# Performance work log

Hardware: AMD Instinct MI355X
Metric: run time of the kernel (lower is better)

## Reference

```python
import jax, jax.numpy as jnp
import numpy as np

T = 2048            # flattened tokens (vLLM style)
D = 4096            # hidden_size
NSSM = 128          # ssm_state_size
K = 4               # conv kernel size
G = 8               # n_groups
H = 128             # mamba_num_heads
P = 64              # mamba_head_dim
INTER = H * P       # 8192 = expand * hidden_size
CONV_DIM = INTER + 2 * G * NSSM   # 10240 (x, B, C share the conv)
PROJ = INTER + CONV_DIM + H       # 18560 (z, xBC, dt)
Q = 128             # SSD chunk size
EPS = 1e-5


def setup_inputs() -> dict:
    key = jax.random.key(0)
    ks = jax.random.split(key, 9)
    s = 0.02
    return {
        "hidden_states": jax.random.normal(ks[0], (T, D), jnp.float32),
        "residual": jax.random.normal(ks[1], (T, D), jnp.float32),
        "norm_w": jnp.ones((D,), jnp.float32),
        "in_proj_w": jax.random.normal(ks[2], (PROJ, D), jnp.float32) * s,
        "conv_w": jax.random.normal(ks[3], (CONV_DIM, K), jnp.float32) * 0.2,
        "conv_b": jax.random.normal(ks[4], (CONV_DIM,), jnp.float32) * 0.1,
        "A_log": jnp.log(jax.random.uniform(ks[5], (H,), jnp.float32, 1.0, 16.0)),
        "D_res": jax.random.normal(ks[6], (H,), jnp.float32) * 0.5 + 1.0,
        "dt_bias": jax.random.normal(ks[7], (H,), jnp.float32) * 0.5,
        "gn_w": jnp.ones((INTER,), jnp.float32),
        "out_proj_w": jax.random.normal(ks[8], (D, INTER), jnp.float32) * s,
    }


def _forward(hidden_states, residual, norm_w, in_proj_w, conv_w, conv_b,
             A_log, D_res, dt_bias, gn_w, out_proj_w):
    # ---- fused add + RMSNorm (vLLM RMSNorm(hidden, residual)) ----
    resid = hidden_states + residual
    hs = resid * jax.lax.rsqrt(jnp.mean(resid * resid, -1, keepdims=True) + EPS) * norm_w

    # ---- MambaMixer2 ----
    proj = hs @ in_proj_w.T                              # [T, PROJ]
    z, xBC, dt = jnp.split(proj, [INTER, INTER + CONV_DIM], axis=-1)

    # causal depthwise conv1d over time + SiLU
    xp = jnp.pad(xBC, ((K - 1, 0), (0, 0)))
    conv = conv_b + sum(conv_w[:, k] * xp[k:k + T] for k in range(K))
    xBC = jax.nn.silu(conv)

    x, B, C = jnp.split(xBC, [INTER, INTER + G * NSSM], axis=-1)
    x = x.reshape(T, H, P)
    Bh = jnp.repeat(B.reshape(T, G, NSSM), H // G, axis=1)   # [T,H,N]
    Ch = jnp.repeat(C.reshape(T, G, NSSM), H // G, axis=1)   # [T,H,N]

    dt = jax.nn.softplus(dt + dt_bias)                   # [T,H]
    A = -jnp.exp(A_log)                                  # [H] (negative)

    # ---- SSD chunked selective scan ----
    NC = T // Q
    a = (dt * A).reshape(NC, Q, H)                       # per-step log decay (<=0)
    cum = jnp.cumsum(a, axis=1)                          # inclusive cumsum, [NC,Q,H]
    Xd = (dt[:, :, None] * x).reshape(NC, Q, H, P)
    Bc = Bh.reshape(NC, Q, H, NSSM)
    Cc = Ch.reshape(NC, Q, H, NSSM)

    # intra-chunk: Y[i] = sum_{j<=i} (C_i.B_j) exp(cum_i-cum_j) Xd_j
    CB = jnp.einsum('cqhn,ckhn->chqk', Cc, Bc)
    cumT = cum.transpose(0, 2, 1)                        # [NC,H,Q]
    mask = jnp.tril(jnp.ones((Q, Q), bool))
    Lm = jnp.where(mask, jnp.exp(cumT[:, :, :, None] - cumT[:, :, None, :]), 0.0)
    Y = jnp.einsum('chqk,ckhp->cqhp', CB * Lm, Xd)

    # chunk-local end states, then scan states across chunks
    cum_end = cum[:, -1]                                 # [NC,H]
    decay_out = jnp.exp(cum_end[:, None] - cum)          # [NC,Q,H]
    S_loc = jnp.einsum('cqhn,cqh,cqhp->chnp', Bc, decay_out, Xd)
    chunk_decay = jnp.exp(cum_end)                       # [NC,H]

    def step(s, inp):
        dec, sl = inp
        return dec[:, None, None] * s + sl, s            # emit state BEFORE chunk

    _, S_prev = jax.lax.scan(step, jnp.zeros((H, NSSM, P), x.dtype),
                             (chunk_decay, S_loc))       # [NC,H,N,P]

    # inter-chunk contribution + skip connection D*x
    Y = Y + jnp.einsum('cqhn,cqh,chnp->cqhp', Cc, jnp.exp(cum), S_prev)
    y = Y.reshape(T, H, P) + D_res[None, :, None] * x

    # gated RMSNorm then out projection
    y = y.reshape(T, INTER) * jax.nn.silu(z)
    y = y * jax.lax.rsqrt(jnp.mean(y * y, -1, keepdims=True) + EPS) * gn_w
    return y @ out_proj_w.T, resid


def reference(hidden_states, residual, norm_w, in_proj_w, conv_w, conv_b,
              A_log, D_res, dt_bias, gn_w, out_proj_w):
    return _forward(hidden_states, residual, norm_w, in_proj_w, conv_w, conv_b,
                    A_log, D_res, dt_bias, gn_w, out_proj_w)
```

## Files before the change

### kernel.cpp

```cpp
#include <hip/hip_runtime.h>
#include <stdint.h>

typedef unsigned short u16;
typedef unsigned int   u32;
typedef float  f32x4  __attribute__((ext_vector_type(4)));
typedef __bf16 bf16x8 __attribute__((ext_vector_type(8)));
typedef u16    u16x4  __attribute__((ext_vector_type(4)));
typedef u16    u16x8  __attribute__((ext_vector_type(8)));

#define T_N     2048
#define D_N     4096
#define H_N     128
#define P_N     64
#define G_N     8
#define NS_N    128
#define INTER_N 8192
#define CONVD_N 10240
#define PROJ_N  18560
#define NGEMM_N 18432
#define NC_N    16

__device__ __forceinline__ float bf2f(u16 u){ u32 x = ((u32)u) << 16; return __builtin_bit_cast(float, x); }
__device__ __forceinline__ u16 f2bf(float f){
  u32 u = __builtin_bit_cast(u32, f);
  u += 0x7FFFu + ((u >> 16) & 1u);
  return (u16)(u >> 16);
}

__device__ __forceinline__ void gld_lds16(const void* g, void* lds){
  __builtin_amdgcn_global_load_lds(
      (const __attribute__((address_space(1))) void*)(uintptr_t)g,
      (__attribute__((address_space(3))) void*)(u32)(uintptr_t)lds,
      16, 0, 0);
}

__global__ __launch_bounds__(256)
void k_addnorm(const float* __restrict__ hin, const float* __restrict__ rin,
               const float* __restrict__ nw, float* __restrict__ resid,
               u16* __restrict__ hs16, float* __restrict__ rstd){
  __shared__ float red[4];
  const int row = blockIdx.x, tid = threadIdx.x;
  const size_t rb = (size_t)row * D_N;
  f32x4 s[4];
  float ss = 0.f;
  #pragma unroll
  for (int i = 0; i < 4; ++i){
    int c4 = tid + i*256;
    f32x4 a = *(const f32x4*)&hin[rb + (size_t)c4*4];
    f32x4 b = *(const f32x4*)&rin[rb + (size_t)c4*4];
    s[i] = a + b;
    *(f32x4*)&resid[rb + (size_t)c4*4] = s[i];
    ss += s[i][0]*s[i][0] + s[i][1]*s[i][1] + s[i][2]*s[i][2] + s[i][3]*s[i][3];
  }
  #pragma unroll
  for (int o = 32; o > 0; o >>= 1) ss += __shfl_down(ss, o, 64);
  if ((tid & 63) == 0) red[tid >> 6] = ss;
  __syncthreads();
  float tot = (red[0] + red[1]) + (red[2] + red[3]);
  float rs = rsqrtf(tot / (float)D_N + 1e-5f);
  if (tid == 0) rstd[row] = rs;
  #pragma unroll
  for (int i = 0; i < 4; ++i){
    int c4 = tid + i*256;
    f32x4 w = *(const f32x4*)&nw[(size_t)c4*4];
    u16x4 o = { f2bf(s[i][0]*rs*w[0]), f2bf(s[i][1]*rs*w[1]),
                f2bf(s[i][2]*rs*w[2]), f2bf(s[i][3]*rs*w[3]) };
    *(u16x4*)&hs16[rb + (size_t)c4*4] = o;
  }
}

__global__ void k_cvt(const float* __restrict__ in, u16* __restrict__ out, size_t n4){
  size_t i = (size_t)blockIdx.x * blockDim.x + threadIdx.x;
  size_t stride = (size_t)gridDim.x * blockDim.x;
  for (; i < n4; i += stride){
    f32x4 v = *(const f32x4*)&in[i*4];
    u16x4 o = { f2bf(v[0]), f2bf(v[1]), f2bf(v[2]), f2bf(v[3]) };
    *(u16x4*)&out[i*4] = o;
  }
}

__global__ void k_wdt(const float* __restrict__ W, const float* __restrict__ nw,
                      float* __restrict__ Wn){
  int idx = blockIdx.x*256 + threadIdx.x;
  int d = idx >> 7, h = idx & 127;
  Wn[(size_t)d*128 + h] = W[(size_t)(INTER_N + CONVD_N + h)*D_N + d] * nw[d];
}

__global__ __launch_bounds__(256)
void k_dtgemm(const float* __restrict__ resid, const float* __restrict__ Wn,
              float* __restrict__ dtpart){
  __shared__ float lhs[16*128];
  const int tid = threadIdx.x;
  const int tb = blockIdx.x >> 3, ks = blockIdx.x & 7;
  const int t0 = tb * 16;
  const int k0 = ks * (D_N / 8);
  const int hcol = tid & 127, rh = tid >> 7;
  float acc[8] = {0,0,0,0,0,0,0,0};
  for (int kt = k0; kt < k0 + D_N/8; kt += 128){
    __syncthreads();
    #pragma unroll
    for (int it = 0; it < 2; ++it){
      int idx = it*256 + tid;
      int rr = idx >> 5, c4 = idx & 31;
      *(f32x4*)&lhs[rr*128 + c4*4] = *(const f32x4*)&resid[(size_t)(t0+rr)*D_N + kt + c4*4];
    }
    __syncthreads();
    #pragma unroll 4
    for (int kk4 = 0; kk4 < 32; ++kk4){
      f32x4 w4;
      #pragma unroll
      for (int j = 0; j < 4; ++j) w4[j] = Wn[(size_t)(kt + kk4*4 + j)*128 + hcol];
      #pragma unroll
      for (int j = 0; j < 8; ++j){
        f32x4 lv = *(const f32x4*)&lhs[(rh*8 + j)*128 + kk4*4];
        acc[j] += lv[0]*w4[0] + lv[1]*w4[1] + lv[2]*w4[2] + lv[3]*w4[3];
      }
    }
  }
  #pragma unroll
  for (int j = 0; j < 8; ++j){
    int t = t0 + rh*8 + j;
    dtpart[((size_t)ks*T_N + t)*128 + hcol] = acc[j];
  }
}

__global__ void k_dtprep(const float* __restrict__ dtpart, const float* __restrict__ rstd,
                         const float* __restrict__ dt_bias, const float* __restrict__ A_log,
                         float* __restrict__ dtv, float* __restrict__ cum,
                         float* __restrict__ cumend, float* __restrict__ dec){
  int c = blockIdx.x, h = threadIdx.x;
  float A = -expf(A_log[h]);
  float bias = dt_bias[h];
  float cm = 0.f;
  for (int q = 0; q < 128; ++q){
    int t = c*128 + q;
    float s = 0.f;
    #pragma unroll
    for (int kspl = 0; kspl < 8; ++kspl)
      s += dtpart[((size_t)kspl*T_N + t)*128 + h];
    float x = s * rstd[t] + bias;
    float dv = (x > 20.f) ? x : log1pf(expf(x));
    dtv[(size_t)t*128 + h] = dv;
    cm += dv * A;
    cum[(size_t)t*128 + h] = cm;
  }
  cumend[c*128 + h] = cm;
  dec[c*128 + h] = expf(cm);
}

#define STA(BUF,HH,KT) gld_lds16(pA + (size_t)((HH)*64)*K + (size_t)(KT)*64, shb + (BUF)*BSZ + (HH)*8192 + tid*16)
#define STB(BUF,HH,KT) gld_lds16(pB[HH] + (size_t)(KT)*64, shb + (BUF)*BSZ + 32768 + (HH)*8192 + tid*16)
#define VMWN do { asm volatile("s_waitcnt vmcnt(%0)" :: "n"(NFRAG) : "memory"); __builtin_amdgcn_sched_barrier(0); } while(0)
#define RDA(BUF, Q, V0, V1, V2, V3)                                                     \
    bf16x8 V0 = *(const bf16x8*)(shb + (BUF)*BSZ + rdA + (Q)*4096 + sA0);               \
    bf16x8 V1 = *(const bf16x8*)(shb + (BUF)*BSZ + rdA + (Q)*4096 + sA1);               \
    bf16x8 V2 = *(const bf16x8*)(shb + (BUF)*BSZ + rdA + (Q)*4096 + 2048 + sA0);        \
    bf16x8 V3 = *(const bf16x8*)(shb + (BUF)*BSZ + rdA + (Q)*4096 + 2048 + sA1);
#define RDB(BUF, BB)                                                                    \
    _Pragma("unroll") for (int nn = 0; nn < NFRAG; ++nn){                               \
      BB[nn][0] = *(const bf16x8*)(shb + (BUF)*BSZ + rdB + nn*2048 + sA0);              \
      BB[nn][1] = *(const bf16x8*)(shb + (BUF)*BSZ + rdB + nn*2048 + sA1);              \
    }
#define MM8(Q, V0, V1, V2, V3, BB)                                                      \
    _Pragma("unroll") for (int nn = 0; nn < NFRAG; ++nn){                               \
      acc[(Q)*2+0][nn] = __builtin_amdgcn_mfma_f32_16x16x32_bf16(V0, BB[nn][0], acc[(Q)*2+0][nn],0,0,0); \
      acc[(Q)*2+0][nn] = __builtin_amdgcn_mfma_f32_16x16x32_bf16(V1, BB[nn][1], acc[(Q)*2+0][nn],0,0,0); \
      acc[(Q)*2+1][nn] = __builtin_amdgcn_mfma_f32_16x16x32_bf16(V2, BB[nn][0], acc[(Q)*2+1][nn],0,0,0); \
      acc[(Q)*2+1][nn] = __builtin_amdgcn_mfma_f32_16x16x32_bf16(V3, BB[nn][1], acc[(Q)*2+1][nn],0,0,0); \
    }
#define ENDPH                                                                           \
    __builtin_amdgcn_s_setprio(0);                                                      \
    __builtin_amdgcn_s_barrier();                                                       \
    __builtin_amdgcn_sched_barrier(0);

template<int NFRAG, typename OT>
__global__ __launch_bounds__(512, 2)
void k_gemm256(const u16* __restrict__ A, const u16* __restrict__ Bm,
               OT* __restrict__ C, int ldc, int K, int nkt, size_t zstride){
  constexpr int BSZ = 32768 + NFRAG*8192;
  __shared__ char shb[2*BSZ];
  const int tid = threadIdx.x, ln = tid & 63, wid = tid >> 6;
  const int wm = wid >> 2, wn = wid & 3;
  const int lr = ln & 15, lg = ln >> 4;

  const int gx = gridDim.x;
  const int lin = blockIdx.y * gx + blockIdx.x;
  const int xcd = lin & 7, sub = lin >> 3;
  const int ncx = gx >> 3;
  const int m0 = (sub / ncx) << 8;
  const int n0 = (xcd * ncx + (sub % ncx)) * (NFRAG*64);
  const int kbase = blockIdx.z * nkt;

  const int srow = tid >> 3;
  const int slog = ((tid & 7) ^ (srow & 7)) * 8;
  const u16* pA = A + (size_t)(m0 + srow)*K + (size_t)kbase*64 + slog;
  const u16* pB[NFRAG];
  #pragma unroll
  for (int hh = 0; hh < NFRAG; ++hh)
    pB[hh] = Bm + (size_t)(n0 + hh*64 + srow)*K + (size_t)kbase*64 + slog;

  const int sA0 = (lg ^ (ln & 7)) << 4;
  const int sA1 = ((4 + lg) ^ (ln & 7)) << 4;
  const u32 rdA = wm*16384 + lr*128;
  const u32 rdB = 32768 + (wn*NFRAG*16 + lr)*128;

  f32x4 acc[8][NFRAG] = {};

  #pragma unroll
  for (int hh = 0; hh < 4; ++hh) STA(0, hh, 0);
  #pragma unroll
  for (int hh = 0; hh < NFRAG; ++hh) STB(0, hh, 0);
  #pragma unroll
  for (int hh = 0; hh < NFRAG; ++hh) STB(1, hh, 1);
  VMWN;
  __builtin_amdgcn_s_barrier();
  __builtin_amdgcn_sched_barrier(0);

  const int nit = nkt >> 1;
  #pragma unroll 1
  for (int it = 0; it < nit; ++it){
    const int t1 = 2*it + 1;
    int t2 = 2*it + 2; if (t2 >= nkt) t2 = 0;
    int t3 = 2*it + 3; if (t3 >= nkt) t3 = 1;
    bf16x8 bb0[NFRAG][2], bb1[NFRAG][2];
    {
      RDA(0,0, x0,x1,x2,x3) RDA(0,1, y0,y1,y2,y3) RDB(0, bb0)
      #pragma unroll
      for (int hh = 0; hh < 4; ++hh) STA(1, hh, t1);
      __builtin_amdgcn_s_setprio(1);
      MM8(0, x0,x1,x2,x3, bb0)
      MM8(1, y0,y1,y2,y3, bb0)
      ENDPH
    }
    {
      RDA(0,2, x0,x1,x2,x3) RDA(0,3, y0,y1,y2,y3)
      #pragma unroll
      for (int hh = 0; hh < NFRAG; ++hh) STB(0, hh, t2);
      VMWN;
      __builtin_amdgcn_s_setprio(1);
      MM8(2, x0,x1,x2,x3, bb0)
      MM8(3, y0,y1,y2,y3, bb0)
      ENDPH
    }
    {
      RDA(1,0, x0,x1,x2,x3) RDA(1,1, y0,y1,y2,y3) RDB(1, bb1)
      #pragma unroll
      for (int hh = 0; hh < 4; ++hh) STA(0, hh, t2);
      __builtin_amdgcn_s_setprio(1);
      MM8(0, x0,x1,x2,x3, bb1)
      MM8(1, y0,y1,y2,y3, bb1)
      ENDPH
    }
    {
      RDA(1,2, x0,x1,x2,x3) RDA(1,3, y0,y1,y2,y3)
      #pragma unroll
      for (int hh = 0; hh < NFRAG; ++hh) STB(1, hh, t3);
      VMWN;
      __builtin_amdgcn_s_setprio(1);
      MM8(2, x0,x1,x2,x3, bb1)
      MM8(3, y0,y1,y2,y3, bb1)
      ENDPH
    }
  }
  asm volatile("s_waitcnt vmcnt(0)" ::: "memory");

  OT* Cz = C + (size_t)blockIdx.z * zstride;
  const int crow = m0 + wm*128 + lg*4;
  const int ccol = n0 + wn*(NFRAG*16) + lr;
  #pragma unroll
  for (int m = 0; m < 8; ++m)
    #pragma unroll
    for (int nn = 0; nn < NFRAG; ++nn)
      #pragma unroll
      for (int r = 0; r < 4; ++r){
        float v = acc[m][nn][r];
        if constexpr (__is_same(OT, float))
          Cz[(size_t)(crow + m*16 + r)*ldc + ccol + nn*16] = v;
        else
          Cz[(size_t)(crow + m*16 + r)*ldc + ccol + nn*16] = f2bf(v);
      }
}

__global__ __launch_bounds__(256)
void k_add2(const float* __restrict__ a, const float* __restrict__ b,
            float* __restrict__ o, int n4){
  int i = blockIdx.x*256 + threadIdx.x;
  if (i < n4){
    f32x4 x = *(const f32x4*)&a[(size_t)i*4];
    f32x4 y = *(const f32x4*)&b[(size_t)i*4];
    x = x + y;
    *(f32x4*)&o[(size_t)i*4] = x;
  }
}

__global__ __launch_bounds__(256)
void k_conv(const u16* __restrict__ proj16, const float* __restrict__ cw,
            const float* __restrict__ cb, u16* __restrict__ x16,
            u16* __restrict__ B16, u16* __restrict__ C16){
  const int ch = blockIdx.x*256 + threadIdx.x;
  const int tbase = blockIdx.y*64;
  f32x4 w = *(const f32x4*)&cw[(size_t)ch*4];
  const float bias = cb[ch];
  const u16* pcol = proj16 + INTER_N + ch;
  float p0 = 0.f, p1 = 0.f, p2 = 0.f;
  if (tbase >= 3){
    p0 = bf2f(pcol[(size_t)(tbase-3)*PROJ_N]);
    p1 = bf2f(pcol[(size_t)(tbase-2)*PROJ_N]);
    p2 = bf2f(pcol[(size_t)(tbase-1)*PROJ_N]);
  }
  u16* xdst = (ch < INTER_N) ? x16 + ch
            : (ch < INTER_N + 1024) ? B16 + (ch - INTER_N)
            : C16 + (ch - INTER_N - 1024);
  const int dstride = (ch < INTER_N) ? INTER_N : 1024;
  #pragma unroll 4
  for (int i = 0; i < 64; ++i){
    int t = tbase + i;
    float cur = bf2f(pcol[(size_t)t*PROJ_N]);
    float acc = bias + w[0]*p0 + w[1]*p1 + w[2]*p2 + w[3]*cur;
    float v = acc / (1.f + __expf(-acc));
    xdst[(size_t)t*dstride] = f2bf(v);
    p0 = p1; p1 = p2; p2 = cur;
  }
}

__global__ __launch_bounds__(512)
void k_ssda(const u16* __restrict__ B16, const u16* __restrict__ x16,
            const float* __restrict__ dtv, const float* __restrict__ cum,
            const float* __restrict__ cumend, u16* __restrict__ SlocT){
  __shared__ u16 lBdT[128*136];
  __shared__ u16 lXdT[64*136];
  __shared__ float lDec[128], lDt[128];
  const int tid = threadIdx.x, wid = tid >> 6, ln = tid & 63;
  const int c = blockIdx.x >> 7, h = blockIdx.x & 127, g = h >> 4;
  if (tid < 128){
    int t = c*128 + tid;
    lDec[tid] = __expf(cumend[c*128 + h] - cum[(size_t)t*128 + h]);
    lDt[tid]  = dtv[(size_t)t*128 + h];
  }
  __syncthreads();
  for (int it = 0; it < 32; ++it){
    int idx = it*512 + tid;
    int q = idx >> 7, n = idx & 127;
    float bv = bf2f(B16[(size_t)(c*128 + q)*1024 + g*128 + n]) * lDec[q];
    lBdT[n*136 + q] = f2bf(bv);
  }
  for (int it = 0; it < 16; ++it){
    int idx = it*512 + tid;
    int q = idx >> 6, p = idx & 63;
    float xv = bf2f(x16[(size_t)(c*128 + q)*INTER_N + h*64 + p]) * lDt[q];
    lXdT[p*136 + q] = f2bf(xv);
  }
  __syncthreads();
  const int wr = wid >> 1, wc = wid & 1;
  const int kofs = (ln >> 4) << 3;
  f32x4 acc[2][2] = {};
  #pragma unroll
  for (int ks = 0; ks < 4; ++ks){
    bf16x8 a[2], b[2];
    #pragma unroll
    for (int m = 0; m < 2; ++m) a[m] = *(const bf16x8*)&lBdT[(wr*32 + m*16 + (ln & 15))*136 + ks*32 + kofs];
    #pragma unroll
    for (int n = 0; n < 2; ++n) b[n] = *(const bf16x8*)&lXdT[(wc*32 + n*16 + (ln & 15))*136 + ks*32 + kofs];
    #pragma unroll
    for (int m = 0; m < 2; ++m)
      #pragma unroll
      for (int n = 0; n < 2; ++n)
        acc[m][n] = __builtin_amdgcn_mfma_f32_16x16x32_bf16(a[m], b[n], acc[m][n], 0, 0, 0);
  }
  const size_t base = (size_t)(c*128 + h) * 8192;
  #pragma unroll
  for (int m = 0; m < 2; ++m)
    #pragma unroll
    for (int n = 0; n < 2; ++n){
      int p  = wc*32 + n*16 + (ln & 15);
      int nn = wr*32 + m*16 + ((ln >> 4) << 2);
      u16x4 o = { f2bf(acc[m][n][0]), f2bf(acc[m][n][1]), f2bf(acc[m][n][2]), f2bf(acc[m][n][3]) };
      *(u16x4*)&SlocT[base + (size_t)p*128 + nn] = o;
    }
}

__global__ __launch_bounds__(256)
void k_scan(const u16* __restrict__ SlocT, const float* __restrict__ dec,
            u16* __restrict__ SprevT){
  int idx = blockIdx.x*256 + threadIdx.x;
  int h = idx >> 11, p = (idx >> 5) & 63, n4 = idx & 31;
  float s0 = 0.f, s1 = 0.f, s2 = 0.f, s3 = 0.f;
  for (int c = 0; c < NC_N; ++c){
    size_t off = (size_t)(c*128 + h)*8192 + (size_t)p*128 + n4*4;
    u16x4 o = { f2bf(s0), f2bf(s1), f2bf(s2), f2bf(s3) };
    *(u16x4*)&SprevT[off] = o;
    u16x4 sl = *(const u16x4*)&SlocT[off];
    float d = dec[c*128 + h];
    s0 = d*s0 + bf2f(sl[0]); s1 = d*s1 + bf2f(sl[1]);
    s2 = d*s2 + bf2f(sl[2]); s3 = d*s3 + bf2f(sl[3]);
  }
}

__global__ __launch_bounds__(512)
void k_ssdb(const u16* __restrict__ C16, const u16* __restrict__ B16g,
            const u16* __restrict__ x16, const float* __restrict__ dtv,
            const float* __restrict__ cum, const u16* __restrict__ SprevT,
            const u16* __restrict__ proj16, const float* __restrict__ Dres,
            u16* __restrict__ yg16){
  __shared__ u16 lC[128*136];
  __shared__ u16 lBP[128*136];
  __shared__ u16 lXdT[64*136];
  __shared__ float lCum[128], lDt[128];
  const int tid = threadIdx.x, wid = tid >> 6, ln = tid & 63;
  const int c = blockIdx.x >> 7, h = blockIdx.x & 127, g = h >> 4;
  if (tid < 128){
    int t = c*128 + tid;
    lCum[tid] = cum[(size_t)t*128 + h];
    lDt[tid]  = dtv[(size_t)t*128 + h];
  }
  __syncthreads();
  for (int it = 0; it < 32; ++it){
    int idx = it*512 + tid;
    int q = idx >> 7, n = idx & 127;
    size_t gi = (size_t)(c*128 + q)*1024 + g*128 + n;
    lC[q*136 + n]  = C16[gi];
    lBP[q*136 + n] = B16g[gi];
  }
  for (int it = 0; it < 16; ++it){
    int idx = it*512 + tid;
    int q = idx >> 6, p = idx & 63;
    lXdT[p*136 + q] = f2bf(bf2f(x16[(size_t)(c*128 + q)*INTER_N + h*64 + p]) * lDt[q]);
  }
  __syncthreads();
  const int kofs = (ln >> 4) << 3;
  {
    const int wr = wid >> 2, wc = wid & 3;
    f32x4 cb[4][2] = {};
    #pragma unroll
    for (int ks = 0; ks < 4; ++ks){
      bf16x8 a[4], b[2];
      #pragma unroll
      for (int m = 0; m < 4; ++m) a[m] = *(const bf16x8*)&lC[(wr*64 + m*16 + (ln & 15))*136 + ks*32 + kofs];
      #pragma unroll
      for (int n = 0; n < 2; ++n) b[n] = *(const bf16x8*)&lBP[(wc*32 + n*16 + (ln & 15))*136 + ks*32 + kofs];
      #pragma unroll
      for (int m = 0; m < 4; ++m)
        #pragma unroll
        for (int n = 0; n < 2; ++n)
          cb[m][n] = __builtin_amdgcn_mfma_f32_16x16x32_bf16(a[m], b[n], cb[m][n], 0, 0, 0);
    }
    __syncthreads();
    #pragma unroll
    for (int m = 0; m < 4; ++m)
      #pragma unroll
      for (int n = 0; n < 2; ++n){
        int kcol = (wid & 3)*32 + n*16 + (ln & 15);
        float ck = lCum[kcol];
        #pragma unroll
        for (int r = 0; r < 4; ++r){
          int q = (wid >> 2)*64 + m*16 + ((ln >> 4) << 2) + r;
          float v = (kcol <= q) ? cb[m][n][r] * __expf(lCum[q] - ck) : 0.f;
          lBP[q*136 + kcol] = f2bf(v);
        }
      }
  }
  __syncthreads();
  const int yr = wid >> 1, yc = wid & 1;
  f32x4 y1[2][2] = {}, y2[2][2] = {};
  const size_t spbase = (size_t)(c*128 + h) * 8192;
  #pragma unroll
  for (int ks = 0; ks < 4; ++ks){
    bf16x8 ap[2], acf[2], bx[2], bs[2];
    #pragma unroll
    for (int m = 0; m < 2; ++m){
      int qr = yr*32 + m*16 + (ln & 15);
      ap[m]  = *(const bf16x8*)&lBP[qr*136 + ks*32 + kofs];
      acf[m] = *(const bf16x8*)&lC [qr*136 + ks*32 + kofs];
    }
    #pragma unroll
    for (int n = 0; n < 2; ++n){
      int p = yc*32 + n*16 + (ln & 15);
      bx[n] = *(const bf16x8*)&lXdT[p*136 + ks*32 + kofs];
      bs[n] = *(const bf16x8*)&SprevT[spbase + (size_t)p*128 + ks*32 + kofs];
    }
    #pragma unroll
    for (int m = 0; m < 2; ++m)
      #pragma unroll
      for (int n = 0; n < 2; ++n){
        y1[m][n] = __builtin_amdgcn_mfma_f32_16x16x32_bf16(ap[m],  bx[n], y1[m][n], 0, 0, 0);
        y2[m][n] = __builtin_amdgcn_mfma_f32_16x16x32_bf16(acf[m], bs[n], y2[m][n], 0, 0, 0);
      }
  }
  const float dh = Dres[h];
  #pragma unroll
  for (int m = 0; m < 2; ++m)
    #pragma unroll
    for (int r = 0; r < 4; ++r){
      int q = yr*32 + m*16 + ((ln >> 4) << 2) + r;
      float eq = __expf(lCum[q]);
      size_t t = (size_t)(c*128 + q);
      #pragma unroll
      for (int n = 0; n < 2; ++n){
        int p = yc*32 + n*16 + (ln & 15);
        int chn = h*64 + p;
        float xv = bf2f(x16[t*INTER_N + chn]);
        float zv = bf2f(proj16[t*PROJ_N + chn]);
        float yv = y1[m][n][r] + eq*y2[m][n][r] + dh*xv;
        float sg = zv / (1.f + __expf(-zv));
        yg16[t*INTER_N + chn] = f2bf(yv * sg);
      }
    }
}

__global__ __launch_bounds__(256)
void k_gnorm(const u16* __restrict__ yg, const float* __restrict__ gnw,
             u16* __restrict__ yn16){
  __shared__ float red[4];
  const int row = blockIdx.x, tid = threadIdx.x;
  const u16* rp = yg + (size_t)row * INTER_N;
  u16x8 v[4];
  float ss = 0.f;
  #pragma unroll
  for (int i = 0; i < 4; ++i){
    v[i] = *(const u16x8*)&rp[(size_t)(tid + i*256)*8];
    #pragma unroll
    for (int j = 0; j < 8; ++j){ float f = bf2f(v[i][j]); ss += f*f; }
  }
  #pragma unroll
  for (int o = 32; o > 0; o >>= 1) ss += __shfl_down(ss, o, 64);
  if ((tid & 63) == 0) red[tid >> 6] = ss;
  __syncthreads();
  float tot = (red[0] + red[1]) + (red[2] + red[3]);
  float sc = rsqrtf(tot / (float)INTER_N + 1e-5f);
  #pragma unroll
  for (int i = 0; i < 4; ++i){
    int c8 = (tid + i*256)*8;
    u16x8 o;
    #pragma unroll
    for (int j = 0; j < 8; ++j)
      o[j] = f2bf(bf2f(v[i][j]) * sc * gnw[c8 + j]);
    *(u16x8*)&yn16[(size_t)row*INTER_N + c8] = o;
  }
}

extern "C" void kernel_launch(void* const* d_in, const int* in_sizes, int n_in,
                              void* d_out, int out_size, void* d_ws, size_t ws_size,
                              hipStream_t stream){
  (void)in_sizes; (void)n_in; (void)out_size;
  const float* hs_in     = (const float*)d_in[0];
  const float* res_in    = (const float*)d_in[1];
  const float* norm_w    = (const float*)d_in[2];
  const float* in_proj_w = (const float*)d_in[3];
  const float* conv_w    = (const float*)d_in[4];
  const float* conv_b    = (const float*)d_in[5];
  const float* A_log     = (const float*)d_in[6];
  const float* D_res     = (const float*)d_in[7];
  const float* dt_bias   = (const float*)d_in[8];
  const float* gn_w      = (const float*)d_in[9];
  const float* out_proj_w= (const float*)d_in[10];

  float* out0      = (float*)d_out;
  float* resid_out = out0 + (size_t)T_N * D_N;

  char* ws = (char*)d_ws;
  const size_t o_hs16   = 0;
  const size_t o_Win16  = 16777216;
  const size_t o_Wout16 = 168820736;
  const size_t o_proj   = 235929600;
  const size_t o_plane  = 311951360;
  const size_t o_Wn     = 387973120;
  const size_t o_dtv    = 391118848;
  const size_t o_cum    = 392167424;
  const size_t o_cumend = 393216000;
  const size_t o_dec    = 393224192;
  const size_t o_rstd   = 393232384;
  const size_t o_x16    = 393240576;
  const size_t o_B16    = 426795008;
  const size_t o_C16    = 430989312;
  const size_t o_SlocT  = 435183616;
  const size_t o_SprevT = 468738048;
  const size_t o_yn16   = 502292480;
  const size_t WS_NEED  = 535846912;
  if (ws_size < WS_NEED) return;

  u16*   hs16   = (u16*)  (ws + o_hs16);
  u16*   Win16  = (u16*)  (ws + o_Win16);
  u16*   Wout16 = (u16*)  (ws + o_Wout16);
  u16*   proj16 = (u16*)  (ws + o_proj);
  float* planes = (float*)(ws + o_plane);
  float* Wn     = (float*)(ws + o_Wn);
  float* dtpart = (float*)(ws + o_proj);
  float* dtv    = (float*)(ws + o_dtv);
  float* cum    = (float*)(ws + o_cum);
  float* cumend = (float*)(ws + o_cumend);
  float* dec    = (float*)(ws + o_dec);
  float* rstd   = (float*)(ws + o_rstd);
  u16*   x16    = (u16*)  (ws + o_x16);
  u16*   B16    = (u16*)  (ws + o_B16);
  u16*   C16    = (u16*)  (ws + o_C16);
  u16*   SlocT  = (u16*)  (ws + o_SlocT);
  u16*   SprevT = (u16*)  (ws + o_SprevT);
  u16*   yn16   = (u16*)  (ws + o_yn16);
  u16*   yg16   = (u16*)  (ws + o_Win16);

  k_addnorm<<<T_N, 256, 0, stream>>>(hs_in, res_in, norm_w, resid_out, hs16, rstd);
  k_cvt<<<4096, 256, 0, stream>>>(in_proj_w,  Win16,  (size_t)NGEMM_N * D_N / 4);
  k_cvt<<<2048, 256, 0, stream>>>(out_proj_w, Wout16, (size_t)D_N * INTER_N / 4);
  k_wdt<<<2048, 256, 0, stream>>>(in_proj_w, norm_w, Wn);
  k_dtgemm<<<1024, 256, 0, stream>>>(resid_out, Wn, dtpart);
  k_dtprep<<<NC_N, 128, 0, stream>>>(dtpart, rstd, dt_bias, A_log, dtv, cum, cumend, dec);
  k_gemm256<3, u16><<<dim3(NGEMM_N/192, T_N/256, 1), 512, 0, stream>>>(hs16, Win16, proj16, PROJ_N, D_N, D_N/64, 0);
  k_conv<<<dim3(CONVD_N/256, T_N/64), 256, 0, stream>>>(proj16, conv_w, conv_b, x16, B16, C16);
  k_ssda<<<NC_N * H_N, 512, 0, stream>>>(B16, x16, dtv, cum, cumend, SlocT);
  k_scan<<<1024, 256, 0, stream>>>(SlocT, dec, SprevT);
  k_ssdb<<<NC_N * H_N, 512, 0, stream>>>(C16, B16, x16, dtv, cum, SprevT, proj16, D_res, yg16);
  k_gnorm<<<T_N, 256, 0, stream>>>(yg16, gn_w, yn16);
  k_gemm256<4, float><<<dim3(D_N/256, T_N/256, 2), 512, 0, stream>>>(yn16, Wout16, planes, D_N, INTER_N, INTER_N/64/2, (size_t)T_N*D_N);
  k_add2<<<T_N*D_N/1024, 256, 0, stream>>>(planes, planes + (size_t)T_N*D_N, out0, T_N*D_N/4);
}
```

Baseline: 952.6 us.

## Shrink GEMM tiles to 128 rows and drop split-K for out projection

The shared GEMM kernel's M tile drops from 256 to 128 rows, which halves the A staging in LDS and the accumulator registers, and the occupancy hint rises from 2 to 4 blocks. The output projection no longer uses split-K with two fp32 partial planes and a separate add kernel. It now runs as a single pass with NFRAG=2 (128x128 tiles) and writes straight to the output. The aim is more blocks in flight and no extra plane writes or reduction kernel, at the cost of less data reuse per tile and more A/B reloads.

```diff
diff --git a/kernel.cpp b/kernel.cpp
--- a/kernel.cpp
+++ b/kernel.cpp
@@ -149,7 +149,7 @@
 }
 
 #define STA(BUF,HH,KT) gld_lds16(pA + (size_t)((HH)*64)*K + (size_t)(KT)*64, shb + (BUF)*BSZ + (HH)*8192 + tid*16)
-#define STB(BUF,HH,KT) gld_lds16(pB[HH] + (size_t)(KT)*64, shb + (BUF)*BSZ + 32768 + (HH)*8192 + tid*16)
+#define STB(BUF,HH,KT) gld_lds16(pB[HH] + (size_t)(KT)*64, shb + (BUF)*BSZ + 16384 + (HH)*8192 + tid*16)
 #define VMWN do { asm volatile("s_waitcnt vmcnt(%0)" :: "n"(NFRAG) : "memory"); __builtin_amdgcn_sched_barrier(0); } while(0)
 #define RDA(BUF, Q, V0, V1, V2, V3)                                                     \
     bf16x8 V0 = *(const bf16x8*)(shb + (BUF)*BSZ + rdA + (Q)*4096 + sA0);               \
@@ -174,10 +174,10 @@
     __builtin_amdgcn_sched_barrier(0);
 
 template<int NFRAG, typename OT>
-__global__ __launch_bounds__(512, 2)
+__global__ __launch_bounds__(512, 4)
 void k_gemm256(const u16* __restrict__ A, const u16* __restrict__ Bm,
-               OT* __restrict__ C, int ldc, int K, int nkt, size_t zstride){
-  constexpr int BSZ = 32768 + NFRAG*8192;
+               OT* __restrict__ C, int ldc, int K, int nkt){
+  constexpr int BSZ = 16384 + NFRAG*8192;
   __shared__ char shb[2*BSZ];
   const int tid = threadIdx.x, ln = tid & 63, wid = tid >> 6;
   const int wm = wid >> 2, wn = wid & 3;
@@ -187,27 +187,25 @@
   const int lin = blockIdx.y * gx + blockIdx.x;
   const int xcd = lin & 7, sub = lin >> 3;
   const int ncx = gx >> 3;
-  const int m0 = (sub / ncx) << 8;
+  const int m0 = (sub / ncx) << 7;
   const int n0 = (xcd * ncx + (sub % ncx)) * (NFRAG*64);
-  const int kbase = blockIdx.z * nkt;
 
   const int srow = tid >> 3;
   const int slog = ((tid & 7) ^ (srow & 7)) * 8;
-  const u16* pA = A + (size_t)(m0 + srow)*K + (size_t)kbase*64 + slog;
+  const u16* pA = A + (size_t)(m0 + srow)*K + slog;
   const u16* pB[NFRAG];
   #pragma unroll
   for (int hh = 0; hh < NFRAG; ++hh)
-    pB[hh] = Bm + (size_t)(n0 + hh*64 + srow)*K + (size_t)kbase*64 + slog;
+    pB[hh] = Bm + (size_t)(n0 + hh*64 + srow)*K + slog;
 
   const int sA0 = (lg ^ (ln & 7)) << 4;
   const int sA1 = ((4 + lg) ^ (ln & 7)) << 4;
-  const u32 rdA = wm*16384 + lr*128;
-  const u32 rdB = 32768 + (wn*NFRAG*16 + lr)*128;
-
-  f32x4 acc[8][NFRAG] = {};
-
-  #pragma unroll
-  for (int hh = 0; hh < 4; ++hh) STA(0, hh, 0);
+  const u32 rdA = wm*8192 + lr*128;
+  const u32 rdB = 16384 + (wn*NFRAG*16 + lr)*128;
+
+  f32x4 acc[4][NFRAG] = {};
+
+  STA(0, 0, 0); STA(0, 1, 0);
   #pragma unroll
   for (int hh = 0; hh < NFRAG; ++hh) STB(0, hh, 0);
   #pragma unroll
@@ -224,73 +222,54 @@
     int t3 = 2*it + 3; if (t3 >= nkt) t3 = 1;
     bf16x8 bb0[NFRAG][2], bb1[NFRAG][2];
     {
-      RDA(0,0, x0,x1,x2,x3) RDA(0,1, y0,y1,y2,y3) RDB(0, bb0)
-      #pragma unroll
-      for (int hh = 0; hh < 4; ++hh) STA(1, hh, t1);
+      RDA(0,0, x0,x1,x2,x3) RDB(0, bb0)
+      STA(1, 0, t1); STA(1, 1, t1);
       __builtin_amdgcn_s_setprio(1);
       MM8(0, x0,x1,x2,x3, bb0)
-      MM8(1, y0,y1,y2,y3, bb0)
       ENDPH
     }
     {
-      RDA(0,2, x0,x1,x2,x3) RDA(0,3, y0,y1,y2,y3)
+      RDA(0,1, x0,x1,x2,x3)
       #pragma unroll
       for (int hh = 0; hh < NFRAG; ++hh) STB(0, hh, t2);
       VMWN;
       __builtin_amdgcn_s_setprio(1);
-      MM8(2, x0,x1,x2,x3, bb0)
-      MM8(3, y0,y1,y2,y3, bb0)
+      MM8(1, x0,x1,x2,x3, bb0)
       ENDPH
     }
     {
-      RDA(1,0, x0,x1,x2,x3) RDA(1,1, y0,y1,y2,y3) RDB(1, bb1)
-      #pragma unroll
-      for (int hh = 0; hh < 4; ++hh) STA(0, hh, t2);
+      RDA(1,0, x0,x1,x2,x3) RDB(1, bb1)
+      STA(0, 0, t2); STA(0, 1, t2);
       __builtin_amdgcn_s_setprio(1);
       MM8(0, x0,x1,x2,x3, bb1)
-      MM8(1, y0,y1,y2,y3, bb1)
       ENDPH
     }
     {
-      RDA(1,2, x0,x1,x2,x3) RDA(1,3, y0,y1,y2,y3)
+      RDA(1,1, x0,x1,x2,x3)
       #pragma unroll
       for (int hh = 0; hh < NFRAG; ++hh) STB(1, hh, t3);
       VMWN;
       __builtin_amdgcn_s_setprio(1);
-      MM8(2, x0,x1,x2,x3, bb1)
-      MM8(3, y0,y1,y2,y3, bb1)
+      MM8(1, x0,x1,x2,x3, bb1)
       ENDPH
     }
   }
   asm volatile("s_waitcnt vmcnt(0)" ::: "memory");
 
-  OT* Cz = C + (size_t)blockIdx.z * zstride;
-  const int crow = m0 + wm*128 + lg*4;
+  const int crow = m0 + wm*64 + lg*4;
   const int ccol = n0 + wn*(NFRAG*16) + lr;
   #pragma unroll
-  for (int m = 0; m < 8; ++m)
+  for (int m = 0; m < 4; ++m)
     #pragma unroll
     for (int nn = 0; nn < NFRAG; ++nn)
       #pragma unroll
       for (int r = 0; r < 4; ++r){
         float v = acc[m][nn][r];
         if constexpr (__is_same(OT, float))
-          Cz[(size_t)(crow + m*16 + r)*ldc + ccol + nn*16] = v;
+          C[(size_t)(crow + m*16 + r)*ldc + ccol + nn*16] = v;
         else
-          Cz[(size_t)(crow + m*16 + r)*ldc + ccol + nn*16] = f2bf(v);
+          C[(size_t)(crow + m*16 + r)*ldc + ccol + nn*16] = f2bf(v);
       }
-}
-
-__global__ __launch_bounds__(256)
-void k_add2(const float* __restrict__ a, const float* __restrict__ b,
-            float* __restrict__ o, int n4){
-  int i = blockIdx.x*256 + threadIdx.x;
-  if (i < n4){
-    f32x4 x = *(const f32x4*)&a[(size_t)i*4];
-    f32x4 y = *(const f32x4*)&b[(size_t)i*4];
-    x = x + y;
-    *(f32x4*)&o[(size_t)i*4] = x;
-  }
 }
 
 __global__ __launch_bounds__(256)
@@ -562,7 +541,6 @@
   const size_t o_Win16  = 16777216;
   const size_t o_Wout16 = 168820736;
   const size_t o_proj   = 235929600;
-  const size_t o_plane  = 311951360;
   const size_t o_Wn     = 387973120;
   const size_t o_dtv    = 391118848;
   const size_t o_cum    = 392167424;
@@ -582,7 +560,6 @@
   u16*   Win16  = (u16*)  (ws + o_Win16);
   u16*   Wout16 = (u16*)  (ws + o_Wout16);
   u16*   proj16 = (u16*)  (ws + o_proj);
-  float* planes = (float*)(ws + o_plane);
   float* Wn     = (float*)(ws + o_Wn);
   float* dtpart = (float*)(ws + o_proj);
   float* dtv    = (float*)(ws + o_dtv);
@@ -604,12 +581,11 @@
   k_wdt<<<2048, 256, 0, stream>>>(in_proj_w, norm_w, Wn);
   k_dtgemm<<<1024, 256, 0, stream>>>(resid_out, Wn, dtpart);
   k_dtprep<<<NC_N, 128, 0, stream>>>(dtpart, rstd, dt_bias, A_log, dtv, cum, cumend, dec);
-  k_gemm256<3, u16><<<dim3(NGEMM_N/192, T_N/256, 1), 512, 0, stream>>>(hs16, Win16, proj16, PROJ_N, D_N, D_N/64, 0);
+  k_gemm256<3, u16><<<dim3(NGEMM_N/192, T_N/128), 512, 0, stream>>>(hs16, Win16, proj16, PROJ_N, D_N, D_N/64);
   k_conv<<<dim3(CONVD_N/256, T_N/64), 256, 0, stream>>>(proj16, conv_w, conv_b, x16, B16, C16);
   k_ssda<<<NC_N * H_N, 512, 0, stream>>>(B16, x16, dtv, cum, cumend, SlocT);
   k_scan<<<1024, 256, 0, stream>>>(SlocT, dec, SprevT);
   k_ssdb<<<NC_N * H_N, 512, 0, stream>>>(C16, B16, x16, dtv, cum, SprevT, proj16, D_res, yg16);
   k_gnorm<<<T_N, 256, 0, stream>>>(yg16, gn_w, yn16);
-  k_gemm256<4, float><<<dim3(D_N/256, T_N/256, 2), 512, 0, stream>>>(yn16, Wout16, planes, D_N, INTER_N, INTER_N/64/2, (size_t)T_N*D_N);
-  k_add2<<<T_N*D_N/1024, 256, 0, stream>>>(planes, planes + (size_t)T_N*D_N, out0, T_N*D_N/4);
-}
+  k_gemm256<2, float><<<dim3(D_N/128, T_N/128), 512, 0, stream>>>(yn16, Wout16, out0, D_N, INTER_N, INTER_N/64);
+}
```

Result: no change. 947.4 us (-0.5%).

## Replace 256-wide GEMM with 256x128 tile, K=32 step, 4-wave kernel

Applied to the files above, without the earlier changes.

Both bf16 GEMMs move from a 512-thread kernel with 256xN (N=192/256) tiles and K-step 64 to a 256-thread kernel with 256x128 tiles and K-step 32, using smaller LDS buffers and a new swizzle and block remapping. The intent is higher occupancy and more blocks per GEMM for better CU balance, at the cost of lower arithmetic intensity per tile and twice as many barriers per K. The out-projection split-K planes now alias the proj workspace, which is no longer needed by then.

```diff
diff --git a/kernel.cpp b/kernel.cpp
--- a/kernel.cpp
+++ b/kernel.cpp
@@ -148,73 +148,58 @@
   dec[c*128 + h] = expf(cm);
 }
 
-#define STA(BUF,HH,KT) gld_lds16(pA + (size_t)((HH)*64)*K + (size_t)(KT)*64, shb + (BUF)*BSZ + (HH)*8192 + tid*16)
-#define STB(BUF,HH,KT) gld_lds16(pB[HH] + (size_t)(KT)*64, shb + (BUF)*BSZ + 32768 + (HH)*8192 + tid*16)
-#define VMWN do { asm volatile("s_waitcnt vmcnt(%0)" :: "n"(NFRAG) : "memory"); __builtin_amdgcn_sched_barrier(0); } while(0)
-#define RDA(BUF, Q, V0, V1, V2, V3)                                                     \
-    bf16x8 V0 = *(const bf16x8*)(shb + (BUF)*BSZ + rdA + (Q)*4096 + sA0);               \
-    bf16x8 V1 = *(const bf16x8*)(shb + (BUF)*BSZ + rdA + (Q)*4096 + sA1);               \
-    bf16x8 V2 = *(const bf16x8*)(shb + (BUF)*BSZ + rdA + (Q)*4096 + 2048 + sA0);        \
-    bf16x8 V3 = *(const bf16x8*)(shb + (BUF)*BSZ + rdA + (Q)*4096 + 2048 + sA1);
-#define RDB(BUF, BB)                                                                    \
-    _Pragma("unroll") for (int nn = 0; nn < NFRAG; ++nn){                               \
-      BB[nn][0] = *(const bf16x8*)(shb + (BUF)*BSZ + rdB + nn*2048 + sA0);              \
-      BB[nn][1] = *(const bf16x8*)(shb + (BUF)*BSZ + rdB + nn*2048 + sA1);              \
-    }
-#define MM8(Q, V0, V1, V2, V3, BB)                                                      \
-    _Pragma("unroll") for (int nn = 0; nn < NFRAG; ++nn){                               \
-      acc[(Q)*2+0][nn] = __builtin_amdgcn_mfma_f32_16x16x32_bf16(V0, BB[nn][0], acc[(Q)*2+0][nn],0,0,0); \
-      acc[(Q)*2+0][nn] = __builtin_amdgcn_mfma_f32_16x16x32_bf16(V1, BB[nn][1], acc[(Q)*2+0][nn],0,0,0); \
-      acc[(Q)*2+1][nn] = __builtin_amdgcn_mfma_f32_16x16x32_bf16(V2, BB[nn][0], acc[(Q)*2+1][nn],0,0,0); \
-      acc[(Q)*2+1][nn] = __builtin_amdgcn_mfma_f32_16x16x32_bf16(V3, BB[nn][1], acc[(Q)*2+1][nn],0,0,0); \
-    }
-#define ENDPH                                                                           \
-    __builtin_amdgcn_s_setprio(0);                                                      \
-    __builtin_amdgcn_s_barrier();                                                       \
-    __builtin_amdgcn_sched_barrier(0);
-
-template<int NFRAG, typename OT>
-__global__ __launch_bounds__(512, 2)
-void k_gemm256(const u16* __restrict__ A, const u16* __restrict__ Bm,
-               OT* __restrict__ C, int ldc, int K, int nkt, size_t zstride){
-  constexpr int BSZ = 32768 + NFRAG*8192;
+#define STA(BUF,HH,KT) gld_lds16(pA + (size_t)((HH)*64)*K + (size_t)(KT)*32, shb + (BUF)*BSZ + (HH)*4096 + tid*16)
+#define STB(BUF,HH,KT) gld_lds16(pB + (size_t)((HH)*64)*K + (size_t)(KT)*32, shb + (BUF)*BSZ + 16384 + (HH)*4096 + tid*16)
+#define VMW2 do { asm volatile("s_waitcnt vmcnt(2)" ::: "memory"); __builtin_amdgcn_sched_barrier(0); } while(0)
+#define BAR  do { __builtin_amdgcn_s_barrier(); __builtin_amdgcn_sched_barrier(0); } while(0)
+#define RDAF(BUF, MOFF, AA)                                                             \
+    _Pragma("unroll") for (int mm = 0; mm < 4; ++mm)                                    \
+      AA[mm] = *(const bf16x8*)(shb + (BUF)*BSZ + rdA + ((MOFF)+mm)*1024 + sxor);
+#define RDBF(BUF, BB)                                                                   \
+    _Pragma("unroll") for (int nn = 0; nn < 4; ++nn)                                    \
+      BB[nn] = *(const bf16x8*)(shb + (BUF)*BSZ + rdB + nn*1024 + sxor);
+#define MMQ(MB, AA, BB)                                                                 \
+    _Pragma("unroll") for (int mm = 0; mm < 4; ++mm)                                    \
+      _Pragma("unroll") for (int nn = 0; nn < 4; ++nn)                                  \
+        acc[(MB)*4+mm][nn] = __builtin_amdgcn_mfma_f32_16x16x32_bf16(AA[mm], BB[nn], acc[(MB)*4+mm][nn],0,0,0);
+
+template<typename OT>
+__global__ __launch_bounds__(256, 2)
+void k_gemm32(const u16* __restrict__ A, const u16* __restrict__ Bm,
+              OT* __restrict__ C, int ldc, int K, int nkt, size_t zstride){
+  constexpr int BSZ = 24576;
   __shared__ char shb[2*BSZ];
   const int tid = threadIdx.x, ln = tid & 63, wid = tid >> 6;
-  const int wm = wid >> 2, wn = wid & 3;
+  const int wm = wid >> 1, wn = wid & 1;
   const int lr = ln & 15, lg = ln >> 4;
 
   const int gx = gridDim.x;
+  const int mt = gridDim.y;
   const int lin = blockIdx.y * gx + blockIdx.x;
   const int xcd = lin & 7, sub = lin >> 3;
   const int ncx = gx >> 3;
-  const int m0 = (sub / ncx) << 8;
-  const int n0 = (xcd * ncx + (sub % ncx)) * (NFRAG*64);
-  const int kbase = blockIdx.z * nkt;
-
-  const int srow = tid >> 3;
-  const int slog = ((tid & 7) ^ (srow & 7)) * 8;
-  const u16* pA = A + (size_t)(m0 + srow)*K + (size_t)kbase*64 + slog;
-  const u16* pB[NFRAG];
-  #pragma unroll
-  for (int hh = 0; hh < NFRAG; ++hh)
-    pB[hh] = Bm + (size_t)(n0 + hh*64 + srow)*K + (size_t)kbase*64 + slog;
-
-  const int sA0 = (lg ^ (ln & 7)) << 4;
-  const int sA1 = ((4 + lg) ^ (ln & 7)) << 4;
-  const u32 rdA = wm*16384 + lr*128;
-  const u32 rdB = 32768 + (wn*NFRAG*16 + lr)*128;
-
-  f32x4 acc[8][NFRAG] = {};
-
-  #pragma unroll
-  for (int hh = 0; hh < 4; ++hh) STA(0, hh, 0);
-  #pragma unroll
-  for (int hh = 0; hh < NFRAG; ++hh) STB(0, hh, 0);
-  #pragma unroll
-  for (int hh = 0; hh < NFRAG; ++hh) STB(1, hh, 1);
-  VMWN;
-  __builtin_amdgcn_s_barrier();
-  __builtin_amdgcn_sched_barrier(0);
+  const int n_local = sub / mt;
+  const int m_idx   = sub % mt;
+  const int m0 = m_idx << 8;
+  const int n0 = (xcd * ncx + n_local) << 7;
+  const int kbase = blockIdx.z * nkt * 32;
+
+  const int srow = tid >> 2;
+  const int slog = ((tid & 3) ^ ((tid >> 3) & 3)) * 8;
+  const u16* pA = A + (size_t)(m0 + srow)*K + kbase + slog;
+  const u16* pB = Bm + (size_t)(n0 + srow)*K + kbase + slog;
+
+  const int sxor = (lg ^ ((ln >> 1) & 3)) << 4;
+  const u32 rdA = wm*8192 + lr*64;
+  const u32 rdB = 16384 + wn*4096 + lr*64;
+
+  f32x4 acc[8][4] = {};
+
+  STA(0,0,0); STA(0,1,0); STA(0,2,0); STA(0,3,0);
+  STB(0,0,0); STB(0,1,0);
+  STB(1,0,1); STB(1,1,1);
+  VMW2;
+  BAR;
 
   const int nit = nkt >> 1;
   #pragma unroll 1
@@ -222,55 +207,51 @@
     const int t1 = 2*it + 1;
     int t2 = 2*it + 2; if (t2 >= nkt) t2 = 0;
     int t3 = 2*it + 3; if (t3 >= nkt) t3 = 1;
-    bf16x8 bb0[NFRAG][2], bb1[NFRAG][2];
+    bf16x8 a[4], b0[4], b1[4];
     {
-      RDA(0,0, x0,x1,x2,x3) RDA(0,1, y0,y1,y2,y3) RDB(0, bb0)
-      #pragma unroll
-      for (int hh = 0; hh < 4; ++hh) STA(1, hh, t1);
+      RDAF(0, 0, a) RDBF(0, b0)
+      STA(1,0,t1); STA(1,1,t1); STA(1,2,t1); STA(1,3,t1);
       __builtin_amdgcn_s_setprio(1);
-      MM8(0, x0,x1,x2,x3, bb0)
-      MM8(1, y0,y1,y2,y3, bb0)
-      ENDPH
+      MMQ(0, a, b0)
+      __builtin_amdgcn_s_setprio(0);
+      BAR;
     }
     {
-      RDA(0,2, x0,x1,x2,x3) RDA(0,3, y0,y1,y2,y3)
-      #pragma unroll
-      for (int hh = 0; hh < NFRAG; ++hh) STB(0, hh, t2);
-      VMWN;
+      RDAF(0, 4, a)
+      STB(0,0,t2); STB(0,1,t2);
+      VMW2;
       __builtin_amdgcn_s_setprio(1);
-      MM8(2, x0,x1,x2,x3, bb0)
-      MM8(3, y0,y1,y2,y3, bb0)
-      ENDPH
+      MMQ(1, a, b0)
+      __builtin_amdgcn_s_setprio(0);
+      BAR;
     }
     {
-      RDA(1,0, x0,x1,x2,x3) RDA(1,1, y0,y1,y2,y3) RDB(1, bb1)
-      #pragma unroll
-      for (int hh = 0; hh < 4; ++hh) STA(0, hh, t2);
+      RDAF(1, 0, a) RDBF(1, b1)
+      STA(0,0,t2); STA(0,1,t2); STA(0,2,t2); STA(0,3,t2);
       __builtin_amdgcn_s_setprio(1);
-      MM8(0, x0,x1,x2,x3, bb1)
-      MM8(1, y0,y1,y2,y3, bb1)
-      ENDPH
+      MMQ(0, a, b1)
+      __builtin_amdgcn_s_setprio(0);
+      BAR;
     }
     {
-      RDA(1,2, x0,x1,x2,x3) RDA(1,3, y0,y1,y2,y3)
-      #pragma unroll
-      for (int hh = 0; hh < NFRAG; ++hh) STB(1, hh, t3);
-      VMWN;
+      RDAF(1, 4, a)
+      STB(1,0,t3); STB(1,1,t3);
+      VMW2;
       __builtin_amdgcn_s_setprio(1);
-      MM8(2, x0,x1,x2,x3, bb1)
-      MM8(3, y0,y1,y2,y3, bb1)
-      ENDPH
+      MMQ(1, a, b1)
+      __builtin_amdgcn_s_setprio(0);
+      BAR;
     }
   }
   asm volatile("s_waitcnt vmcnt(0)" ::: "memory");
 
   OT* Cz = C + (size_t)blockIdx.z * zstride;
   const int crow = m0 + wm*128 + lg*4;
-  const int ccol = n0 + wn*(NFRAG*16) + lr;
+  const int ccol = n0 + wn*64 + lr;
   #pragma unroll
   for (int m = 0; m < 8; ++m)
     #pragma unroll
-    for (int nn = 0; nn < NFRAG; ++nn)
+    for (int nn = 0; nn < 4; ++nn)
       #pragma unroll
       for (int r = 0; r < 4; ++r){
         float v = acc[m][nn][r];
@@ -562,7 +543,6 @@
   const size_t o_Win16  = 16777216;
   const size_t o_Wout16 = 168820736;
   const size_t o_proj   = 235929600;
-  const size_t o_plane  = 311951360;
   const size_t o_Wn     = 387973120;
   const size_t o_dtv    = 391118848;
   const size_t o_cum    = 392167424;
@@ -582,9 +562,9 @@
   u16*   Win16  = (u16*)  (ws + o_Win16);
   u16*   Wout16 = (u16*)  (ws + o_Wout16);
   u16*   proj16 = (u16*)  (ws + o_proj);
-  float* planes = (float*)(ws + o_plane);
   float* Wn     = (float*)(ws + o_Wn);
   float* dtpart = (float*)(ws + o_proj);
+  float* planes = (float*)(ws + o_proj);
   float* dtv    = (float*)(ws + o_dtv);
   float* cum    = (float*)(ws + o_cum);
   float* cumend = (float*)(ws + o_cumend);
@@ -604,12 +584,12 @@
   k_wdt<<<2048, 256, 0, stream>>>(in_proj_w, norm_w, Wn);
   k_dtgemm<<<1024, 256, 0, stream>>>(resid_out, Wn, dtpart);
   k_dtprep<<<NC_N, 128, 0, stream>>>(dtpart, rstd, dt_bias, A_log, dtv, cum, cumend, dec);
-  k_gemm256<3, u16><<<dim3(NGEMM_N/192, T_N/256, 1), 512, 0, stream>>>(hs16, Win16, proj16, PROJ_N, D_N, D_N/64, 0);
+  k_gemm32<u16><<<dim3(NGEMM_N/128, T_N/256, 1), 256, 0, stream>>>(hs16, Win16, proj16, PROJ_N, D_N, D_N/32, 0);
   k_conv<<<dim3(CONVD_N/256, T_N/64), 256, 0, stream>>>(proj16, conv_w, conv_b, x16, B16, C16);
   k_ssda<<<NC_N * H_N, 512, 0, stream>>>(B16, x16, dtv, cum, cumend, SlocT);
   k_scan<<<1024, 256, 0, stream>>>(SlocT, dec, SprevT);
   k_ssdb<<<NC_N * H_N, 512, 0, stream>>>(C16, B16, x16, dtv, cum, SprevT, proj16, D_res, yg16);
   k_gnorm<<<T_N, 256, 0, stream>>>(yg16, gn_w, yn16);
-  k_gemm256<4, float><<<dim3(D_N/256, T_N/256, 2), 512, 0, stream>>>(yn16, Wout16, planes, D_N, INTER_N, INTER_N/64/2, (size_t)T_N*D_N);
+  k_gemm32<float><<<dim3(D_N/128, T_N/256, 2), 256, 0, stream>>>(yn16, Wout16, planes, D_N, INTER_N, INTER_N/32/2, (size_t)T_N*D_N);
   k_add2<<<T_N*D_N/1024, 256, 0, stream>>>(planes, planes + (size_t)T_N*D_N, out0, T_N*D_N/4);
 }
```

New measurement: 1.030 ms. 1.08x slower.
